# Performance work log

Hardware: AMD Instinct MI355X
Metric: run time of the kernel (lower is better)

Reference implementation:

```python
import jax, jax.numpy as jnp
import numpy as np

L = 256            # model length (match states)
Q = 2 * L + 3      # num_states = 2*length + 3
M = 1              # num_models
B = 256            # batch of sequences
T = 512            # sequence length (timesteps)
EPS = 1e-16


def setup_inputs() -> dict:
    key = jax.random.key(0)
    k1, k2, k3 = jax.random.split(key, 3)
    return {
        "emission_probs": jax.random.uniform(k1, (T, M, B, Q), dtype=jnp.float32),
        "log_A": jax.random.normal(k2, (M, Q, Q), dtype=jnp.float32),
        "init_logits": jax.random.normal(k3, (M, Q), dtype=jnp.float32),
    }


def reference(emission_probs, log_A, init_logits):
    # Dense transition matrix per model (row-stochastic), as in transitioner.make_log_A()
    A = jax.nn.softmax(log_A, axis=-1)                 # (M, Q, Q)
    init_dist = jax.nn.softmax(init_logits, axis=-1)   # (M, Q)

    def norm_step(E, R, ll):
        # One scaled-forward update: multiply emission, normalize, accumulate loglik.
        E = jnp.maximum(E, EPS)
        R = jnp.maximum(R, EPS)
        a = E * R                                      # (M, B, Q)
        S = jnp.sum(a, axis=-1, keepdims=True)         # (M, B, 1)
        ll = ll + jnp.log(S)
        a = a / S
        return a, ll

    # t = 0: init=True -> R is the initial distribution (no transition applied)
    R0 = jnp.broadcast_to(init_dist[:, None, :], (M, B, Q))
    fwd0, ll0 = norm_step(emission_probs[0], R0, jnp.zeros((M, B, 1), jnp.float32))
    out0 = jnp.concatenate([jnp.log(fwd0), ll0], axis=-1)  # (M, B, Q+1)

    def step(carry, E_t):
        fwd, ll = carry
        # transitioner(old_scaled_forward): dense transition matvec per model
        R = jnp.einsum('mbq,mqk->mbk', fwd, A)
        a, ll = norm_step(E_t, R, ll)
        return (a, ll), jnp.concatenate([jnp.log(a), ll], axis=-1)

    _, outs = jax.lax.scan(step, (fwd0, ll0), emission_probs[1:])
    outs = jnp.concatenate([out0[None], outs], axis=0)     # (T, M, B, Q+1)
    # RNN output layout: (M*B, T, Q+1)
    return jnp.transpose(outs, (1, 2, 0, 3)).reshape(M * B, T, Q + 1)
```

## Files before the change

### kernel.cpp

```cpp
#include <hip/hip_runtime.h>
#include <cstdint>

typedef unsigned long long u64;
typedef float f32x4 __attribute__((ext_vector_type(4)));
typedef short s16x4 __attribute__((ext_vector_type(4)));

#define Qn   515
#define QP   520
#define Bn   256
#define Tn   512
#define OQ   516
#define EPSc 1e-16f
#define NSL  65
#define NT   5
#define KT   33
#define KTA  17
#define QPW  528
#define USTR 532
#define NGRP 32
#define NBLK 8

#define WS_AMATH 0
#define WS_INIT  565760
#define WS_FBUF  568320
#define WS_TOTAL (WS_FBUF + 2162688)

#define L_FRAG 0
#define L_UST  (NT*KT*64*8)
#define LDS_TOTAL (L_UST + 16*USTR*2 + 16)

__device__ __forceinline__ unsigned bfbits(float x) {
    unsigned u = __builtin_bit_cast(unsigned, x);
    unsigned r = u + 0x7FFFu + ((u >> 16) & 1u);
    return r >> 16;
}

__global__ void prep_A(const float* __restrict__ logA, unsigned* __restrict__ AMATh) {
    __shared__ float red[4];
    __shared__ float srow[Qn];
    int row = blockIdx.x, tid = threadIdx.x;
    if (row >= Qn) {
        for (int c = tid; c < 260; c += 256) AMATh[(size_t)row*260 + c] = 0u;
        return;
    }
    float mx = -1e30f;
    for (int c = tid; c < Qn; c += 256) { float x = logA[(size_t)row*Qn + c]; srow[c] = x; mx = fmaxf(mx, x); }
#pragma unroll
    for (int o = 32; o > 0; o >>= 1) mx = fmaxf(mx, __shfl_xor(mx, o));
    if ((tid & 63) == 0) red[tid >> 6] = mx;
    __syncthreads();
    mx = fmaxf(fmaxf(red[0], red[1]), fmaxf(red[2], red[3]));
    __syncthreads();
    float sm = 0.f;
    for (int c = tid; c < Qn; c += 256) sm += __expf(srow[c] - mx);
#pragma unroll
    for (int o = 32; o > 0; o >>= 1) sm += __shfl_xor(sm, o);
    if ((tid & 63) == 0) red[tid >> 6] = sm;
    __syncthreads();
    float inv = 1.f / (red[0] + red[1] + red[2] + red[3]);
    for (int c2 = tid; c2 < 260; c2 += 256) {
        int c = 2*c2;
        float v0 = (c   < Qn) ? __expf(srow[c]   - mx) * inv : 0.f;
        float v1 = (c+1 < Qn) ? __expf(srow[c+1] - mx) * inv : 0.f;
        AMATh[(size_t)row*260 + c2] = bfbits(v0) | (bfbits(v1) << 16);
    }
}

__global__ void prep_init(const float* __restrict__ il, float* __restrict__ INITD) {
    __shared__ float red[4];
    __shared__ float srow[Qn];
    int tid = threadIdx.x;
    float mx = -1e30f;
    for (int c = tid; c < Qn; c += 256) { float x = il[c]; srow[c] = x; mx = fmaxf(mx, x); }
#pragma unroll
    for (int o = 32; o > 0; o >>= 1) mx = fmaxf(mx, __shfl_xor(mx, o));
    if ((tid & 63) == 0) red[tid >> 6] = mx;
    __syncthreads();
    mx = fmaxf(fmaxf(red[0], red[1]), fmaxf(red[2], red[3]));
    __syncthreads();
    float sm = 0.f;
    for (int c = tid; c < Qn; c += 256) sm += __expf(srow[c] - mx);
#pragma unroll
    for (int o = 32; o > 0; o >>= 1) sm += __shfl_xor(sm, o);
    if ((tid & 63) == 0) red[tid >> 6] = sm;
    __syncthreads();
    float inv = 1.f / (red[0] + red[1] + red[2] + red[3]);
    for (int c = tid; c < 520; c += 256)
        INITD[c] = (c < Qn) ? __expf(srow[c] - mx) * inv : 0.f;
}

__global__ void __launch_bounds__(256, 1)
hmm_fwd(const float* __restrict__ E, const unsigned* __restrict__ AMATh,
        const float* __restrict__ INITD, float* __restrict__ out,
        u64* __restrict__ fbuf)
{
    extern __shared__ char smem[];
    uint2* frag = (uint2*)(smem + L_FRAG);
    unsigned short* ustage = (unsigned short*)(smem + L_UST);

    const int tid  = threadIdx.x;
    const int lane = tid & 63;
    const int wv   = tid >> 6;
    const int bid  = blockIdx.x;
    const int g    = bid & 31;
    const int j    = bid >> 5;
    const int b0   = g * 8;
    const int q0   = j * NSL;
    const int q0p  = j * 66;

    for (int f = tid; f < NT*KT*64; f += 256) {
        int tile = f >> 6, l = f & 63;
        int nt = tile / KT, kt = tile - nt*KT;
        int col = q0 + nt*16 + (l & 15);
        int kb  = kt*16 + ((l >> 4) << 2);
        unsigned h[4];
#pragma unroll
        for (int i = 0; i < 4; ++i) {
            int pk_ = kb + i;
            int jr = pk_ / 66, rr = pk_ - jr*66;
            unsigned hv = 0;
            if (rr < 65 && col < QP) {
                int qrow = jr*65 + rr;
                unsigned w = AMATh[(size_t)qrow*260 + (col >> 1)];
                hv = (col & 1) ? (w >> 16) : (w & 0xffffu);
            }
            h[i] = hv;
        }
        uint2 pk;
        pk.x = h[0] | (h[1] << 16);
        pk.y = h[2] | (h[3] << 16);
        frag[f] = pk;
    }
    for (int i = tid; i < 16*(USTR/2); i += 256) ((unsigned*)ustage)[i] = 0u;
    __syncthreads();

    const int ntn = (wv == 0) ? 2 : 1;
    const int nts0 = wv;
    int eoff[2][4];
#pragma unroll
    for (int sl = 0; sl < 2; ++sl) {
#pragma unroll
        for (int r = 0; r < 4; ++r) {
            int nt  = sl ? 4 : nts0;
            int row = ((lane >> 4) << 2) + r;
            int col = nt*16 + (lane & 15);
            int q   = q0 + col;
            bool ok = (lane < 32) && (col < NSL) && (q < Qn) && (sl < ntn);
            eoff[sl][r] = ok ? ((b0 + row)*Qn + q) : -1;
        }
    }
    const int rrow = tid >> 5;
    const int t32  = tid & 31;

    float llreg = 0.f;
    float v[17];
    float lsr = 0.f;

    {
        u64* fw = fbuf + ((size_t)0*NGRP + g)*8*QPW;
        for (int p = tid; p < 8*66; p += 256) {
            int row = p / 66, c = p - row*66;
            int q = q0 + c;
            float uv = 0.f;
            if (c < 65 && q < Qn)
                uv = fmaxf(E[(size_t)(b0+row)*Qn + q], EPSc) * fmaxf(INITD[q], EPSc);
            u64 pk = (u64)__builtin_bit_cast(unsigned, uv) | ((u64)1u << 32);
            __hip_atomic_store(&fw[(size_t)row*QPW + q0p + c], pk,
                               __ATOMIC_RELAXED, __HIP_MEMORY_SCOPE_AGENT);
        }
    }

    auto poll_read = [&](int s) {
        const size_t base = ((size_t)((s-1) & 1)*NGRP + g)*8*QPW + (size_t)rrow*QPW;
        const u64* fb = fbuf + base;
        unsigned want = (unsigned)s;
        u64 w[17];
        unsigned pend = (t32 < 16) ? 0x1FFFFu : 0xFFFFu;
        while (true) {
#pragma unroll
            for (int k = 0; k < 17; ++k) {
                if (pend & (1u << k))
                    w[k] = __hip_atomic_load(&fb[t32 + 32*k],
                                             __ATOMIC_RELAXED, __HIP_MEMORY_SCOPE_AGENT);
            }
#pragma unroll
            for (int k = 0; k < 17; ++k)
                if ((pend & (1u << k)) && (unsigned)(w[k] >> 32) == want) pend &= ~(1u << k);
            if (pend == 0) break;
        }
        float sum = 0.f;
#pragma unroll
        for (int k = 0; k < 17; ++k) {
            int pc = t32 + 32*k;
            v[k] = (pc < QPW) ? __builtin_bit_cast(float, (unsigned)(w[k] & 0xffffffffu)) : 0.f;
            sum += v[k];
        }
#pragma unroll
        for (int o = 1; o < 32; o <<= 1) sum += __shfl_xor(sum, o);
        lsr = __logf(sum);
        llreg += lsr;
        return 1.f / sum;
    };

    auto emit_outputs = [&](int tOut) {
        if (j == 0 && t32 == 0)
            out[((size_t)(b0 + rrow)*Tn + tOut)*OQ + Qn] = llreg;
#pragma unroll
        for (int k = 0; k < 17; ++k) {
            int pc = t32 + 32*k;
            int c = pc - q0p;
            if (pc < QPW && c >= 0 && c < 65) {
                int q = q0 + c;
                if (q < Qn)
                    out[((size_t)(b0 + rrow)*Tn + tOut)*OQ + q] = __logf(v[k]) - lsr;
            }
        }
    };

    for (int s = 1; s < Tn; ++s) {
        float ev[2][4];
        size_t ebase = (size_t)s * Bn * Qn;
#pragma unroll
        for (int sl = 0; sl < 2; ++sl)
#pragma unroll
            for (int r = 0; r < 4; ++r)
                ev[sl][r] = (eoff[sl][r] >= 0) ? E[ebase + eoff[sl][r]] : 0.f;

        float inv = poll_read(s);

        __syncthreads();
#pragma unroll
        for (int k = 0; k < 17; ++k) {
            int pc = t32 + 32*k;
            if (pc < QPW)
                ustage[rrow*USTR + pc] = (unsigned short)bfbits(v[k] * inv);
        }
        __syncthreads();

        f32x4 a0a = {0.f,0.f,0.f,0.f}, a0b = {0.f,0.f,0.f,0.f};
        f32x4 a1a = {0.f,0.f,0.f,0.f}, a1b = {0.f,0.f,0.f,0.f};
        {
            const unsigned short* urow = ustage + (lane & 15)*USTR + ((lane >> 4) << 2);
            const uint2* f0 = frag + (size_t)(nts0*KT)*64 + lane;
            const uint2* f1 = frag + (size_t)(4*KT)*64 + lane;
#pragma unroll 2
            for (int kt = 0; kt < KTA; ++kt) {
                s16x4 af = __builtin_bit_cast(s16x4, *(const uint2*)(urow + kt*16));
                a0a = __builtin_amdgcn_mfma_f32_16x16x16bf16_1k(af, __builtin_bit_cast(s16x4, f0[kt*64]), a0a, 0, 0, 0);
                if (ntn == 2)
                    a1a = __builtin_amdgcn_mfma_f32_16x16x16bf16_1k(af, __builtin_bit_cast(s16x4, f1[kt*64]), a1a, 0, 0, 0);
                int k2 = kt + KTA;
                if (k2 < KT) {
                    s16x4 af2 = __builtin_bit_cast(s16x4, *(const uint2*)(urow + k2*16));
                    a0b = __builtin_amdgcn_mfma_f32_16x16x16bf16_1k(af2, __builtin_bit_cast(s16x4, f0[k2*64]), a0b, 0, 0, 0);
                    if (ntn == 2)
                        a1b = __builtin_amdgcn_mfma_f32_16x16x16bf16_1k(af2, __builtin_bit_cast(s16x4, f1[k2*64]), a1b, 0, 0, 0);
                }
            }
        }
        {
            unsigned seqv = (unsigned)(s + 1);
            u64* fw = fbuf + ((size_t)(s & 1)*NGRP + g)*8*QPW;
            if (lane < 32) {
#pragma unroll
                for (int r = 0; r < 4; ++r) {
                    int row = ((lane >> 4) << 2) + r;
                    {
                        int col = nts0*16 + (lane & 15);
                        float R = fmaxf(a0a[r] + a0b[r], EPSc);
                        int q = q0 + col;
                        float uv = (q < Qn) ? fmaxf(ev[0][r], EPSc) * R : 0.f;
                        u64 pk = (u64)__builtin_bit_cast(unsigned, uv) | ((u64)seqv << 32);
                        __hip_atomic_store(&fw[(size_t)row*QPW + q0p + col], pk,
                                           __ATOMIC_RELAXED, __HIP_MEMORY_SCOPE_AGENT);
                    }
                    if (ntn == 2 && (lane & 15) == 0) {
                        int col = 64;
                        float R = fmaxf(a1a[r] + a1b[r], EPSc);
                        int q = q0 + col;
                        float uv = (q < Qn) ? fmaxf(ev[1][r], EPSc) * R : 0.f;
                        u64 pk = (u64)__builtin_bit_cast(unsigned, uv) | ((u64)seqv << 32);
                        __hip_atomic_store(&fw[(size_t)row*QPW + q0p + col], pk,
                                           __ATOMIC_RELAXED, __HIP_MEMORY_SCOPE_AGENT);
                    }
                }
            }
            if (wv == 1 && lane >= 32 && lane < 40) {
                int row = lane - 32;
                u64 pk = ((u64)seqv << 32);
                __hip_atomic_store(&fw[(size_t)row*QPW + q0p + 65], pk,
                                   __ATOMIC_RELAXED, __HIP_MEMORY_SCOPE_AGENT);
            }
        }
        emit_outputs(s - 1);
    }

    poll_read(Tn);
    emit_outputs(Tn - 1);
}

extern "C" void kernel_launch(void* const* d_in, const int* in_sizes, int n_in,
                              void* d_out, int out_size, void* d_ws, size_t ws_size,
                              hipStream_t stream) {
    (void)in_sizes; (void)n_in; (void)out_size;
    if (ws_size < (size_t)WS_TOTAL) return;

    const float* E    = (const float*)d_in[0];
    const float* logA = (const float*)d_in[1];
    const float* il   = (const float*)d_in[2];
    float* out = (float*)d_out;
    char*  ws  = (char*)d_ws;

    unsigned* AMATh = (unsigned*)(ws + WS_AMATH);
    float*    INITD = (float*)(ws + WS_INIT);
    u64*      fbuf  = (u64*)(ws + WS_FBUF);

    prep_A<<<544, 256, 0, stream>>>(logA, AMATh);
    prep_init<<<1, 256, 0, stream>>>(il, INITD);

    static_assert(LDS_TOTAL < 160*1024, "LDS budget");
    hipFuncSetAttribute(reinterpret_cast<const void*>(hmm_fwd),
                        hipFuncAttributeMaxDynamicSharedMemorySize, LDS_TOTAL);
    hmm_fwd<<<256, 256, LDS_TOTAL, stream>>>(E, AMATh, INITD, out, fbuf);
}
```

Baseline: 2.929 ms.

## Replace per-element seq-tagged exchange with bf16 payload plus per-block flags

The inter-block forward-vector exchange used to write a 64-bit word per element, pairing an fp32 value with a sequence tag, and each reader polled every word until all tags matched. Now each block stages its slice in LDS and publishes it as packed bf16 pairs. It then sets one per-block flag, and readers poll only the 8 flags before doing a single bulk load of the payload. This cuts the bytes moved and the polling traffic on the serial 511-step chain. In exchange it adds extra __syncthreads and a dependent flag-then-payload round trip, relies on relaxed atomics for ordering, and computes outputs from bf16-rounded values.

```diff
diff --git a/kernel.cpp b/kernel.cpp
--- a/kernel.cpp
+++ b/kernel.cpp
@@ -1,6 +1,7 @@
 #include <hip/hip_runtime.h>
 #include <cstdint>
 
+typedef unsigned u32t;
 typedef unsigned long long u64;
 typedef float f32x4 __attribute__((ext_vector_type(4)));
 typedef short s16x4 __attribute__((ext_vector_type(4)));
@@ -15,24 +16,33 @@
 #define NT   5
 #define KT   33
 #define KTA  17
-#define QPW  528
 #define USTR 532
 #define NGRP 32
 #define NBLK 8
+#define RWORDS 264
 
 #define WS_AMATH 0
 #define WS_INIT  565760
-#define WS_FBUF  568320
-#define WS_TOTAL (WS_FBUF + 2162688)
+#define WS_PAY   568320
+#define WS_FLG   (WS_PAY + 540672)
+#define WS_TOTAL (WS_FLG + 32768)
 
 #define L_FRAG 0
 #define L_UST  (NT*KT*64*8)
-#define LDS_TOTAL (L_UST + 16*USTR*2 + 16)
+#define L_USL  (L_UST + 16*USTR*2)
+#define L_SIG  (L_USL + 8*68*4)
+#define LDS_TOTAL (L_SIG + 128)
 
 __device__ __forceinline__ unsigned bfbits(float x) {
     unsigned u = __builtin_bit_cast(unsigned, x);
     unsigned r = u + 0x7FFFu + ((u >> 16) & 1u);
     return r >> 16;
+}
+__device__ __forceinline__ float bflo(u32t w) {
+    return __builtin_bit_cast(float, w << 16);
+}
+__device__ __forceinline__ float bfhi(u32t w) {
+    return __builtin_bit_cast(float, w & 0xffff0000u);
 }
 
 __global__ void prep_A(const float* __restrict__ logA, unsigned* __restrict__ AMATh) {
@@ -92,11 +102,15 @@
 __global__ void __launch_bounds__(256, 1)
 hmm_fwd(const float* __restrict__ E, const unsigned* __restrict__ AMATh,
         const float* __restrict__ INITD, float* __restrict__ out,
-        u64* __restrict__ fbuf)
+        u32t* __restrict__ pay, u32t* __restrict__ flg)
 {
     extern __shared__ char smem[];
     uint2* frag = (uint2*)(smem + L_FRAG);
     unsigned short* ustage = (unsigned short*)(smem + L_UST);
+    u32t* ustage32 = (u32t*)ustage;
+    float* usl  = (float*)(smem + L_USL);
+    float* invs = (float*)(smem + L_SIG);
+    float* lsig = invs + 8;
 
     const int tid  = threadIdx.x;
     const int lane = tid & 63;
@@ -106,7 +120,6 @@
     const int j    = bid >> 5;
     const int b0   = g * 8;
     const int q0   = j * NSL;
-    const int q0p  = j * 66;
 
     for (int f = tid; f < NT*KT*64; f += 256) {
         int tile = f >> 6, l = f & 63;
@@ -131,7 +144,7 @@
         pk.y = h[2] | (h[3] << 16);
         frag[f] = pk;
     }
-    for (int i = tid; i < 16*(USTR/2); i += 256) ((unsigned*)ustage)[i] = 0u;
+    for (int i = tid; i < 16*(USTR/2); i += 256) ustage32[i] = 0u;
     __syncthreads();
 
     const int ntn = (wv == 0) ? 2 : 1;
@@ -151,71 +164,107 @@
     }
     const int rrow = tid >> 5;
     const int t32  = tid & 31;
+    const int nw   = (t32 < 8) ? 9 : 8;
 
     float llreg = 0.f;
-    float v[17];
     float lsr = 0.f;
-
-    {
-        u64* fw = fbuf + ((size_t)0*NGRP + g)*8*QPW;
-        for (int p = tid; p < 8*66; p += 256) {
-            int row = p / 66, c = p - row*66;
-            int q = q0 + c;
-            float uv = 0.f;
-            if (c < 65 && q < Qn)
-                uv = fmaxf(E[(size_t)(b0+row)*Qn + q], EPSc) * fmaxf(INITD[q], EPSc);
-            u64 pk = (u64)__builtin_bit_cast(unsigned, uv) | ((u64)1u << 32);
-            __hip_atomic_store(&fw[(size_t)row*QPW + q0p + c], pk,
+    u32t w9[9];
+
+    auto pay_base = [&](int slot) { return pay + ((size_t)slot*NGRP + g)*(8*RWORDS); };
+    auto flg_idx  = [&](int slot, int jj) { return ((unsigned)(slot*NGRP + g)*NBLK + jj)*16; };
+
+    auto publish = [&](int s) {
+        __syncthreads();
+        u32t* pb = pay_base(s & 1);
+        for (int p = tid; p < 8*33; p += 256) {
+            int row = p / 33, c2 = p - row*33;
+            float a0 = usl[row*68 + 2*c2];
+            float a1 = usl[row*68 + 2*c2 + 1];
+            u32t pk = bfbits(a0) | (bfbits(a1) << 16);
+            __hip_atomic_store(&pb[row*RWORDS + 33*j + c2], pk,
                                __ATOMIC_RELAXED, __HIP_MEMORY_SCOPE_AGENT);
         }
-    }
-
-    auto poll_read = [&](int s) {
-        const size_t base = ((size_t)((s-1) & 1)*NGRP + g)*8*QPW + (size_t)rrow*QPW;
-        const u64* fb = fbuf + base;
+        __syncthreads();
+        if (tid == 0)
+            __hip_atomic_store(&flg[flg_idx(s & 1, j)], (u32t)(s + 1),
+                               __ATOMIC_RELAXED, __HIP_MEMORY_SCOPE_AGENT);
+    };
+
+    auto poll_flags = [&](int s) {
+        const u32t* fb = flg + flg_idx((s - 1) & 1, 0);
         unsigned want = (unsigned)s;
-        u64 w[17];
-        unsigned pend = (t32 < 16) ? 0x1FFFFu : 0xFFFFu;
         while (true) {
-#pragma unroll
-            for (int k = 0; k < 17; ++k) {
-                if (pend & (1u << k))
-                    w[k] = __hip_atomic_load(&fb[t32 + 32*k],
-                                             __ATOMIC_RELAXED, __HIP_MEMORY_SCOPE_AGENT);
-            }
-#pragma unroll
-            for (int k = 0; k < 17; ++k)
-                if ((pend & (1u << k)) && (unsigned)(w[k] >> 32) == want) pend &= ~(1u << k);
-            if (pend == 0) break;
-        }
+            u32t fv = 0xffffffffu;
+            if (lane < 8)
+                fv = __hip_atomic_load(&fb[lane*16], __ATOMIC_RELAXED, __HIP_MEMORY_SCOPE_AGENT);
+            if (__all(fv >= want)) break;
+        }
+    };
+
+    auto bulk_reduce = [&](int s) {
+        const u32t* pb = pay_base((s - 1) & 1) + (size_t)rrow*RWORDS;
+#pragma unroll
+        for (int k = 0; k < 8; ++k)
+            w9[k] = __hip_atomic_load(&pb[t32 + 32*k], __ATOMIC_RELAXED, __HIP_MEMORY_SCOPE_AGENT);
+        w9[8] = (t32 < 8) ? __hip_atomic_load(&pb[256 + t32], __ATOMIC_RELAXED, __HIP_MEMORY_SCOPE_AGENT) : 0u;
         float sum = 0.f;
 #pragma unroll
-        for (int k = 0; k < 17; ++k) {
-            int pc = t32 + 32*k;
-            v[k] = (pc < QPW) ? __builtin_bit_cast(float, (unsigned)(w[k] & 0xffffffffu)) : 0.f;
-            sum += v[k];
+        for (int k = 0; k < 9; ++k) {
+            if (k < nw) { sum += bflo(w9[k]) + bfhi(w9[k]); }
         }
 #pragma unroll
         for (int o = 1; o < 32; o <<= 1) sum += __shfl_xor(sum, o);
         lsr = __logf(sum);
         llreg += lsr;
-        return 1.f / sum;
+        if (t32 == 0) { invs[rrow] = 1.f / sum; lsig[rrow] = lsr; }
+    };
+
+    auto stage = [&]() {
+        float iv = invs[rrow];
+#pragma unroll
+        for (int k = 0; k < 9; ++k) {
+            if (k < nw) {
+                int wi = (k < 8) ? (t32 + 32*k) : (256 + t32);
+                u32t pk = bfbits(bflo(w9[k]) * iv) | (bfbits(bfhi(w9[k]) * iv) << 16);
+                ustage32[rrow*(USTR/2) + wi] = pk;
+            }
+        }
     };
 
     auto emit_outputs = [&](int tOut) {
-        if (j == 0 && t32 == 0)
+        if (t32 == 0 && j == 0)
             out[((size_t)(b0 + rrow)*Tn + tOut)*OQ + Qn] = llreg;
-#pragma unroll
-        for (int k = 0; k < 17; ++k) {
-            int pc = t32 + 32*k;
-            int c = pc - q0p;
-            if (pc < QPW && c >= 0 && c < 65) {
-                int q = q0 + c;
-                if (q < Qn)
-                    out[((size_t)(b0 + rrow)*Tn + tOut)*OQ + q] = __logf(v[k]) - lsr;
-            }
-        }
-    };
+        float* orow = out + ((size_t)(b0 + rrow)*Tn + tOut)*OQ;
+#pragma unroll
+        for (int k = 0; k < 9; ++k) {
+            if (k < nw) {
+                int wi = (k < 8) ? (t32 + 32*k) : (256 + t32);
+                int c0 = 2*wi;
+#pragma unroll
+                for (int h = 0; h < 2; ++h) {
+                    int c = c0 + h;
+                    int jr = c / 66, loc = c - jr*66;
+                    if (jr == j && loc < 65) {
+                        int q = q0 + loc;
+                        if (q < Qn) {
+                            float f = h ? bfhi(w9[k]) : bflo(w9[k]);
+                            orow[q] = __logf(f) - lsr;
+                        }
+                    }
+                }
+            }
+        }
+    };
+
+    for (int p = tid; p < 8*66; p += 256) {
+        int row = p / 66, c = p - row*66;
+        int q = q0 + c;
+        float uv = 0.f;
+        if (c < 65 && q < Qn)
+            uv = fmaxf(E[(size_t)(b0+row)*Qn + q], EPSc) * fmaxf(INITD[q], EPSc);
+        usl[row*68 + c] = uv;
+    }
+    publish(0);
 
     for (int s = 1; s < Tn; ++s) {
         float ev[2][4];
@@ -226,15 +275,10 @@
             for (int r = 0; r < 4; ++r)
                 ev[sl][r] = (eoff[sl][r] >= 0) ? E[ebase + eoff[sl][r]] : 0.f;
 
-        float inv = poll_read(s);
-
+        poll_flags(s);
+        bulk_reduce(s);
         __syncthreads();
-#pragma unroll
-        for (int k = 0; k < 17; ++k) {
-            int pc = t32 + 32*k;
-            if (pc < QPW)
-                ustage[rrow*USTR + pc] = (unsigned short)bfbits(v[k] * inv);
-        }
+        stage();
         __syncthreads();
 
         f32x4 a0a = {0.f,0.f,0.f,0.f}, a0b = {0.f,0.f,0.f,0.f};
@@ -258,44 +302,35 @@
                 }
             }
         }
-        {
-            unsigned seqv = (unsigned)(s + 1);
-            u64* fw = fbuf + ((size_t)(s & 1)*NGRP + g)*8*QPW;
-            if (lane < 32) {
-#pragma unroll
-                for (int r = 0; r < 4; ++r) {
-                    int row = ((lane >> 4) << 2) + r;
-                    {
-                        int col = nts0*16 + (lane & 15);
+        if (lane < 32) {
+#pragma unroll
+            for (int r = 0; r < 4; ++r) {
+                int row = ((lane >> 4) << 2) + r;
+                {
+                    int col = nts0*16 + (lane & 15);
+                    if (col < NSL) {
                         float R = fmaxf(a0a[r] + a0b[r], EPSc);
                         int q = q0 + col;
-                        float uv = (q < Qn) ? fmaxf(ev[0][r], EPSc) * R : 0.f;
-                        u64 pk = (u64)__builtin_bit_cast(unsigned, uv) | ((u64)seqv << 32);
-                        __hip_atomic_store(&fw[(size_t)row*QPW + q0p + col], pk,
-                                           __ATOMIC_RELAXED, __HIP_MEMORY_SCOPE_AGENT);
+                        usl[row*68 + col] = (q < Qn) ? fmaxf(ev[0][r], EPSc) * R : 0.f;
                     }
-                    if (ntn == 2 && (lane & 15) == 0) {
-                        int col = 64;
+                }
+                if (ntn == 2) {
+                    int col = 64 + (lane & 15);
+                    if (col < NSL) {
                         float R = fmaxf(a1a[r] + a1b[r], EPSc);
                         int q = q0 + col;
-                        float uv = (q < Qn) ? fmaxf(ev[1][r], EPSc) * R : 0.f;
-                        u64 pk = (u64)__builtin_bit_cast(unsigned, uv) | ((u64)seqv << 32);
-                        __hip_atomic_store(&fw[(size_t)row*QPW + q0p + col], pk,
-                                           __ATOMIC_RELAXED, __HIP_MEMORY_SCOPE_AGENT);
+                        usl[row*68 + col] = (q < Qn) ? fmaxf(ev[1][r], EPSc) * R : 0.f;
                     }
                 }
             }
-            if (wv == 1 && lane >= 32 && lane < 40) {
-                int row = lane - 32;
-                u64 pk = ((u64)seqv << 32);
-                __hip_atomic_store(&fw[(size_t)row*QPW + q0p + 65], pk,
-                                   __ATOMIC_RELAXED, __HIP_MEMORY_SCOPE_AGENT);
-            }
-        }
+        }
+        publish(s);
+
         emit_outputs(s - 1);
     }
 
-    poll_read(Tn);
+    poll_flags(Tn);
+    bulk_reduce(Tn);
     emit_outputs(Tn - 1);
 }
 
@@ -313,7 +348,10 @@
 
     unsigned* AMATh = (unsigned*)(ws + WS_AMATH);
     float*    INITD = (float*)(ws + WS_INIT);
-    u64*      fbuf  = (u64*)(ws + WS_FBUF);
+    u32t*     pay   = (u32t*)(ws + WS_PAY);
+    u32t*     flgp  = (u32t*)(ws + WS_FLG);
+
+    hipMemsetAsync(ws + WS_FLG, 0, 32768, stream);
 
     prep_A<<<544, 256, 0, stream>>>(logA, AMATh);
     prep_init<<<1, 256, 0, stream>>>(il, INITD);
@@ -321,5 +359,5 @@
     static_assert(LDS_TOTAL < 160*1024, "LDS budget");
     hipFuncSetAttribute(reinterpret_cast<const void*>(hmm_fwd),
                         hipFuncAttributeMaxDynamicSharedMemorySize, LDS_TOTAL);
-    hmm_fwd<<<256, 256, LDS_TOTAL, stream>>>(E, AMATh, INITD, out, fbuf);
-}
+    hmm_fwd<<<256, 256, LDS_TOTAL, stream>>>(E, AMATh, INITD, out, pay, flgp);
+}
```

New measurement: 3.090 ms. +5.5%, slower.

## Pack bf16 pairs in inter-block exchange and give each block two batch chunks

Applied to the files above, without the earlier changes.

The inter-block forward-vector exchange now packs two bf16 values plus a step tag into each 64-bit word, halving the words every block polls and writes. The grid shrinks from 256 to 128 blocks, each handling two 8-row batch chunks with separate LDS staging buffers. One chunk's compute and publish can then overlap other blocks' progress on the other chunk. This is meant to cut cross-block synchronisation and exchange traffic, the dominant per-timestep latency. In exchange, output log-probabilities and normalisers are computed from bf16-rounded values, which loses precision, and a memset of the exchange buffer is added before launch.

```diff
diff --git a/kernel.cpp b/kernel.cpp
--- a/kernel.cpp
+++ b/kernel.cpp
@@ -1,6 +1,7 @@
 #include <hip/hip_runtime.h>
 #include <cstdint>
 
+typedef unsigned u32t;
 typedef unsigned long long u64;
 typedef float f32x4 __attribute__((ext_vector_type(4)));
 typedef short s16x4 __attribute__((ext_vector_type(4)));
@@ -15,25 +16,29 @@
 #define NT   5
 #define KT   33
 #define KTA  17
-#define QPW  528
 #define USTR 532
-#define NGRP 32
+#define GR   16
+#define NCH  2
 #define NBLK 8
+#define RW   264
 
 #define WS_AMATH 0
 #define WS_INIT  565760
 #define WS_FBUF  568320
-#define WS_TOTAL (WS_FBUF + 2162688)
+#define WS_TOTAL (WS_FBUF + 1081344)
 
 #define L_FRAG 0
 #define L_UST  (NT*KT*64*8)
-#define LDS_TOTAL (L_UST + 16*USTR*2 + 16)
+#define USTB   (16*USTR*2)
+#define LDS_TOTAL (L_UST + NCH*USTB + 16)
 
 __device__ __forceinline__ unsigned bfbits(float x) {
     unsigned u = __builtin_bit_cast(unsigned, x);
     unsigned r = u + 0x7FFFu + ((u >> 16) & 1u);
     return r >> 16;
 }
+__device__ __forceinline__ float bflo(u32t w) { return __builtin_bit_cast(float, w << 16); }
+__device__ __forceinline__ float bfhi(u32t w) { return __builtin_bit_cast(float, w & 0xffff0000u); }
 
 __global__ void prep_A(const float* __restrict__ logA, unsigned* __restrict__ AMATh) {
     __shared__ float red[4];
@@ -96,17 +101,15 @@
 {
     extern __shared__ char smem[];
     uint2* frag = (uint2*)(smem + L_FRAG);
-    unsigned short* ustage = (unsigned short*)(smem + L_UST);
+    unsigned short* ustage0 = (unsigned short*)(smem + L_UST);
 
     const int tid  = threadIdx.x;
     const int lane = tid & 63;
     const int wv   = tid >> 6;
     const int bid  = blockIdx.x;
-    const int g    = bid & 31;
-    const int j    = bid >> 5;
-    const int b0   = g * 8;
+    const int g    = bid >> 3;
+    const int j    = bid & 7;
     const int q0   = j * NSL;
-    const int q0p  = j * 66;
 
     for (int f = tid; f < NT*KT*64; f += 256) {
         int tile = f >> 6, l = f & 63;
@@ -131,172 +134,192 @@
         pk.y = h[2] | (h[3] << 16);
         frag[f] = pk;
     }
-    for (int i = tid; i < 16*(USTR/2); i += 256) ((unsigned*)ustage)[i] = 0u;
-    __syncthreads();
-
-    const int ntn = (wv == 0) ? 2 : 1;
+    for (int i = tid; i < NCH*(USTB/4); i += 256) ((u32t*)ustage0)[i] = 0u;
+    __syncthreads();
+
+    const int ntn  = (wv == 0) ? 2 : 1;
     const int nts0 = wv;
-    int eoff[2][4];
-#pragma unroll
-    for (int sl = 0; sl < 2; ++sl) {
-#pragma unroll
-        for (int r = 0; r < 4; ++r) {
-            int nt  = sl ? 4 : nts0;
-            int row = ((lane >> 4) << 2) + r;
-            int col = nt*16 + (lane & 15);
-            int q   = q0 + col;
-            bool ok = (lane < 32) && (col < NSL) && (q < Qn) && (sl < ntn);
-            eoff[sl][r] = ok ? ((b0 + row)*Qn + q) : -1;
+    int eoff[NCH][2][4];
+#pragma unroll
+    for (int c = 0; c < NCH; ++c) {
+        int b0 = g*16 + c*8;
+#pragma unroll
+        for (int sl = 0; sl < 2; ++sl) {
+#pragma unroll
+            for (int r = 0; r < 4; ++r) {
+                int nt  = sl ? 4 : nts0;
+                int row = ((lane >> 4) << 2) + r;
+                int col = nt*16 + (lane & 15);
+                int q   = q0 + col;
+                bool ok = (lane < 32) && (col < NSL) && (q < Qn) && (sl < ntn);
+                eoff[c][sl][r] = ok ? ((b0 + row)*Qn + q) : -1;
+            }
         }
     }
     const int rrow = tid >> 5;
     const int t32  = tid & 31;
-
-    float llreg = 0.f;
-    float v[17];
+    const int nw   = (t32 < 8) ? 9 : 8;
+
+    float llreg[NCH]; llreg[0] = 0.f; llreg[1] = 0.f;
     float lsr = 0.f;
-
-    {
-        u64* fw = fbuf + ((size_t)0*NGRP + g)*8*QPW;
-        for (int p = tid; p < 8*66; p += 256) {
-            int row = p / 66, c = p - row*66;
-            int q = q0 + c;
-            float uv = 0.f;
-            if (c < 65 && q < Qn)
-                uv = fmaxf(E[(size_t)(b0+row)*Qn + q], EPSc) * fmaxf(INITD[q], EPSc);
-            u64 pk = (u64)__builtin_bit_cast(unsigned, uv) | ((u64)1u << 32);
-            __hip_atomic_store(&fw[(size_t)row*QPW + q0p + c], pk,
-                               __ATOMIC_RELAXED, __HIP_MEMORY_SCOPE_AGENT);
-        }
-    }
-
-    auto poll_read = [&](int s) {
-        const size_t base = ((size_t)((s-1) & 1)*NGRP + g)*8*QPW + (size_t)rrow*QPW;
-        const u64* fb = fbuf + base;
-        unsigned want = (unsigned)s;
-        u64 w[17];
-        unsigned pend = (t32 < 16) ? 0x1FFFFu : 0xFFFFu;
-        while (true) {
-#pragma unroll
-            for (int k = 0; k < 17; ++k) {
-                if (pend & (1u << k))
-                    w[k] = __hip_atomic_load(&fb[t32 + 32*k],
-                                             __ATOMIC_RELAXED, __HIP_MEMORY_SCOPE_AGENT);
-            }
-#pragma unroll
-            for (int k = 0; k < 17; ++k)
-                if ((pend & (1u << k)) && (unsigned)(w[k] >> 32) == want) pend &= ~(1u << k);
-            if (pend == 0) break;
+    u64 w9[9];
+
+    auto buf_base = [&](int slot, int c) {
+        return fbuf + (size_t)(((slot*GR + g)*NCH + c)*8) * RW;
+    };
+
+    auto poll_read = [&](int s, int c) -> float {
+        const unsigned want = (unsigned)s;
+        const u64* pb = buf_base((s-1) & 1, c) + (size_t)rrow*RW;
+        unsigned pend = (t32 < 8) ? 0x1FFu : 0xFFu;
+        while (pend) {
+#pragma unroll
+            for (int k = 0; k < 9; ++k) if (pend & (1u << k)) {
+                int wi = (k < 8) ? (t32 + 32*k) : (256 + t32);
+                w9[k] = __hip_atomic_load(&pb[wi], __ATOMIC_RELAXED, __HIP_MEMORY_SCOPE_AGENT);
+            }
+#pragma unroll
+            for (int k = 0; k < 9; ++k)
+                if ((pend & (1u << k)) && (unsigned)(w9[k] >> 32) == want) pend &= ~(1u << k);
         }
         float sum = 0.f;
 #pragma unroll
-        for (int k = 0; k < 17; ++k) {
-            int pc = t32 + 32*k;
-            v[k] = (pc < QPW) ? __builtin_bit_cast(float, (unsigned)(w[k] & 0xffffffffu)) : 0.f;
-            sum += v[k];
-        }
+        for (int k = 0; k < 9; ++k) if (k < nw) { u32t pr = (u32t)w9[k]; sum += bflo(pr) + bfhi(pr); }
 #pragma unroll
         for (int o = 1; o < 32; o <<= 1) sum += __shfl_xor(sum, o);
         lsr = __logf(sum);
-        llreg += lsr;
+        llreg[c] += lsr;
         return 1.f / sum;
     };
 
-    auto emit_outputs = [&](int tOut) {
-        if (j == 0 && t32 == 0)
-            out[((size_t)(b0 + rrow)*Tn + tOut)*OQ + Qn] = llreg;
-#pragma unroll
-        for (int k = 0; k < 17; ++k) {
-            int pc = t32 + 32*k;
-            int c = pc - q0p;
-            if (pc < QPW && c >= 0 && c < 65) {
-                int q = q0 + c;
-                if (q < Qn)
-                    out[((size_t)(b0 + rrow)*Tn + tOut)*OQ + q] = __logf(v[k]) - lsr;
-            }
+    auto stage = [&](float iv, int c) {
+        u32t* us32 = (u32t*)(ustage0) + c*(USTB/4) + rrow*(USTR/2);
+#pragma unroll
+        for (int k = 0; k < 9; ++k) if (k < nw) {
+            int wi = (k < 8) ? (t32 + 32*k) : (256 + t32);
+            u32t pr = (u32t)w9[k];
+            us32[wi] = bfbits(bflo(pr)*iv) | (bfbits(bfhi(pr)*iv) << 16);
         }
     };
 
+    auto emit_outputs = [&](int tOut, int c) {
+        int brow = g*16 + c*8 + rrow;
+        float* orow = out + ((size_t)brow*Tn + tOut)*OQ;
+        if (t32 == 0 && j == 0) orow[Qn] = llreg[c];
+#pragma unroll
+        for (int k = 0; k < 9; ++k) if (k < nw) {
+            int wi = (k < 8) ? (t32 + 32*k) : (256 + t32);
+            u32t pr = (u32t)w9[k];
+            int c0 = 2*wi;
+#pragma unroll
+            for (int h = 0; h < 2; ++h) {
+                int cc = c0 + h;
+                int jr = cc / 66, loc = cc - jr*66;
+                if (jr == j && loc < 65) {
+                    int q = q0 + loc;
+                    if (q < Qn) orow[q] = __logf(h ? bfhi(pr) : bflo(pr)) - lsr;
+                }
+            }
+        }
+    };
+
+#pragma unroll
+    for (int c = 0; c < NCH; ++c) {
+        u64* pp = buf_base(0, c);
+        int b0 = g*16 + c*8;
+        for (int p = tid; p < 264; p += 256) {
+            int row = p/33, c2 = p - row*33;
+            int lc0 = 2*c2, lc1 = lc0 + 1;
+            float v0 = 0.f, v1 = 0.f;
+            int qa = q0 + lc0, qb = q0 + lc1;
+            if (lc0 < 65 && qa < Qn) v0 = fmaxf(E[(size_t)(b0+row)*Qn + qa], EPSc) * fmaxf(INITD[qa], EPSc);
+            if (lc1 < 65 && qb < Qn) v1 = fmaxf(E[(size_t)(b0+row)*Qn + qb], EPSc) * fmaxf(INITD[qb], EPSc);
+            u64 word = (u64)(bfbits(v0) | (bfbits(v1) << 16)) | ((u64)1u << 32);
+            __hip_atomic_store(&pp[(size_t)row*RW + j*33 + c2], word,
+                               __ATOMIC_RELAXED, __HIP_MEMORY_SCOPE_AGENT);
+        }
+    }
+
     for (int s = 1; s < Tn; ++s) {
-        float ev[2][4];
+        float ev[NCH][2][4];
         size_t ebase = (size_t)s * Bn * Qn;
 #pragma unroll
-        for (int sl = 0; sl < 2; ++sl)
-#pragma unroll
-            for (int r = 0; r < 4; ++r)
-                ev[sl][r] = (eoff[sl][r] >= 0) ? E[ebase + eoff[sl][r]] : 0.f;
-
-        float inv = poll_read(s);
-
-        __syncthreads();
-#pragma unroll
-        for (int k = 0; k < 17; ++k) {
-            int pc = t32 + 32*k;
-            if (pc < QPW)
-                ustage[rrow*USTR + pc] = (unsigned short)bfbits(v[k] * inv);
-        }
-        __syncthreads();
-
-        f32x4 a0a = {0.f,0.f,0.f,0.f}, a0b = {0.f,0.f,0.f,0.f};
-        f32x4 a1a = {0.f,0.f,0.f,0.f}, a1b = {0.f,0.f,0.f,0.f};
-        {
-            const unsigned short* urow = ustage + (lane & 15)*USTR + ((lane >> 4) << 2);
-            const uint2* f0 = frag + (size_t)(nts0*KT)*64 + lane;
-            const uint2* f1 = frag + (size_t)(4*KT)*64 + lane;
+        for (int c = 0; c < NCH; ++c)
+#pragma unroll
+            for (int sl = 0; sl < 2; ++sl)
+#pragma unroll
+                for (int r = 0; r < 4; ++r)
+                    ev[c][sl][r] = (eoff[c][sl][r] >= 0) ? E[ebase + eoff[c][sl][r]] : 0.f;
+
+#pragma unroll
+        for (int c = 0; c < NCH; ++c) {
+            float iv = poll_read(s, c);
+            stage(iv, c);
+            __syncthreads();
+
+            f32x4 a0a = {0.f,0.f,0.f,0.f}, a0b = {0.f,0.f,0.f,0.f};
+            f32x4 a1a = {0.f,0.f,0.f,0.f}, a1b = {0.f,0.f,0.f,0.f};
+            {
+                const unsigned short* urow = ustage0 + c*(USTB/2)
+                                           + (lane & 15)*USTR + ((lane >> 4) << 2);
+                const uint2* f0 = frag + (size_t)(nts0*KT)*64 + lane;
+                const uint2* f1 = frag + (size_t)(4*KT)*64 + lane;
 #pragma unroll 2
-            for (int kt = 0; kt < KTA; ++kt) {
-                s16x4 af = __builtin_bit_cast(s16x4, *(const uint2*)(urow + kt*16));
-                a0a = __builtin_amdgcn_mfma_f32_16x16x16bf16_1k(af, __builtin_bit_cast(s16x4, f0[kt*64]), a0a, 0, 0, 0);
-                if (ntn == 2)
-                    a1a = __builtin_amdgcn_mfma_f32_16x16x16bf16_1k(af, __builtin_bit_cast(s16x4, f1[kt*64]), a1a, 0, 0, 0);
-                int k2 = kt + KTA;
-                if (k2 < KT) {
-                    s16x4 af2 = __builtin_bit_cast(s16x4, *(const uint2*)(urow + k2*16));
-                    a0b = __builtin_amdgcn_mfma_f32_16x16x16bf16_1k(af2, __builtin_bit_cast(s16x4, f0[k2*64]), a0b, 0, 0, 0);
+                for (int kt = 0; kt < KTA; ++kt) {
+                    s16x4 af = __builtin_bit_cast(s16x4, *(const uint2*)(urow + kt*16));
+                    a0a = __builtin_amdgcn_mfma_f32_16x16x16bf16_1k(af, __builtin_bit_cast(s16x4, f0[kt*64]), a0a, 0, 0, 0);
                     if (ntn == 2)
-                        a1b = __builtin_amdgcn_mfma_f32_16x16x16bf16_1k(af2, __builtin_bit_cast(s16x4, f1[k2*64]), a1b, 0, 0, 0);
-                }
-            }
-        }
-        {
-            unsigned seqv = (unsigned)(s + 1);
-            u64* fw = fbuf + ((size_t)(s & 1)*NGRP + g)*8*QPW;
-            if (lane < 32) {
-#pragma unroll
-                for (int r = 0; r < 4; ++r) {
-                    int row = ((lane >> 4) << 2) + r;
-                    {
-                        int col = nts0*16 + (lane & 15);
-                        float R = fmaxf(a0a[r] + a0b[r], EPSc);
-                        int q = q0 + col;
-                        float uv = (q < Qn) ? fmaxf(ev[0][r], EPSc) * R : 0.f;
-                        u64 pk = (u64)__builtin_bit_cast(unsigned, uv) | ((u64)seqv << 32);
-                        __hip_atomic_store(&fw[(size_t)row*QPW + q0p + col], pk,
-                                           __ATOMIC_RELAXED, __HIP_MEMORY_SCOPE_AGENT);
-                    }
-                    if (ntn == 2 && (lane & 15) == 0) {
-                        int col = 64;
-                        float R = fmaxf(a1a[r] + a1b[r], EPSc);
-                        int q = q0 + col;
-                        float uv = (q < Qn) ? fmaxf(ev[1][r], EPSc) * R : 0.f;
-                        u64 pk = (u64)__builtin_bit_cast(unsigned, uv) | ((u64)seqv << 32);
-                        __hip_atomic_store(&fw[(size_t)row*QPW + q0p + col], pk,
-                                           __ATOMIC_RELAXED, __HIP_MEMORY_SCOPE_AGENT);
+                        a1a = __builtin_amdgcn_mfma_f32_16x16x16bf16_1k(af, __builtin_bit_cast(s16x4, f1[kt*64]), a1a, 0, 0, 0);
+                    int k2 = kt + KTA;
+                    if (k2 < KT) {
+                        s16x4 af2 = __builtin_bit_cast(s16x4, *(const uint2*)(urow + k2*16));
+                        a0b = __builtin_amdgcn_mfma_f32_16x16x16bf16_1k(af2, __builtin_bit_cast(s16x4, f0[k2*64]), a0b, 0, 0, 0);
+                        if (ntn == 2)
+                            a1b = __builtin_amdgcn_mfma_f32_16x16x16bf16_1k(af2, __builtin_bit_cast(s16x4, f1[k2*64]), a1b, 0, 0, 0);
                     }
                 }
             }
-            if (wv == 1 && lane >= 32 && lane < 40) {
-                int row = lane - 32;
-                u64 pk = ((u64)seqv << 32);
-                __hip_atomic_store(&fw[(size_t)row*QPW + q0p + 65], pk,
-                                   __ATOMIC_RELAXED, __HIP_MEMORY_SCOPE_AGENT);
-            }
-        }
-        emit_outputs(s - 1);
-    }
-
-    poll_read(Tn);
-    emit_outputs(Tn - 1);
+
+            {
+                u64 tagw = ((u64)(unsigned)(s + 1)) << 32;
+                u64* pp = buf_base(s & 1, c);
+                if (lane < 32) {
+#pragma unroll
+                    for (int r = 0; r < 4; ++r) {
+                        int row = ((lane >> 4) << 2) + r;
+                        {
+                            int colLoc = nts0*16 + (lane & 15);
+                            float R = fmaxf(a0a[r] + a0b[r], EPSc);
+                            int q = q0 + colLoc;
+                            float uv = (q < Qn) ? fmaxf(ev[c][0][r], EPSc) * R : 0.f;
+                            float uvn = __shfl_xor(uv, 1);
+                            if (!(lane & 1)) {
+                                int c2 = colLoc >> 1;
+                                u64 word = (u64)(bfbits(uv) | (bfbits(uvn) << 16)) | tagw;
+                                __hip_atomic_store(&pp[(size_t)row*RW + j*33 + c2], word,
+                                                   __ATOMIC_RELAXED, __HIP_MEMORY_SCOPE_AGENT);
+                            }
+                        }
+                        if (ntn == 2 && (lane & 15) == 0) {
+                            float R4 = fmaxf(a1a[r] + a1b[r], EPSc);
+                            int q4 = q0 + 64;
+                            float uv4 = (q4 < Qn) ? fmaxf(ev[c][1][r], EPSc) * R4 : 0.f;
+                            u64 word = (u64)bfbits(uv4) | tagw;
+                            __hip_atomic_store(&pp[(size_t)row*RW + j*33 + 32], word,
+                                               __ATOMIC_RELAXED, __HIP_MEMORY_SCOPE_AGENT);
+                        }
+                    }
+                }
+            }
+            emit_outputs(s - 1, c);
+        }
+    }
+
+#pragma unroll
+    for (int c = 0; c < NCH; ++c) {
+        poll_read(Tn, c);
+        emit_outputs(Tn - 1, c);
+    }
 }
 
 extern "C" void kernel_launch(void* const* d_in, const int* in_sizes, int n_in,
@@ -315,11 +338,13 @@
     float*    INITD = (float*)(ws + WS_INIT);
     u64*      fbuf  = (u64*)(ws + WS_FBUF);
 
+    hipMemsetAsync(ws + WS_FBUF, 0, 1081344, stream);
+
     prep_A<<<544, 256, 0, stream>>>(logA, AMATh);
     prep_init<<<1, 256, 0, stream>>>(il, INITD);
 
     static_assert(LDS_TOTAL < 160*1024, "LDS budget");
     hipFuncSetAttribute(reinterpret_cast<const void*>(hmm_fwd),
                         hipFuncAttributeMaxDynamicSharedMemorySize, LDS_TOTAL);
-    hmm_fwd<<<256, 256, LDS_TOTAL, stream>>>(E, AMATh, INITD, out, fbuf);
-}
+    hmm_fwd<<<GR*NBLK, 256, LDS_TOTAL, stream>>>(E, AMATh, INITD, out, fbuf);
+}
```

Measured after the change: 6.248 ms. 2.13x slower.
